# Performance work log

Hardware: AMD Instinct MI355X
Metric: run time of the kernel (lower is better)

Reference implementation:

```python
import jax, jax.numpy as jnp
import numpy as np

N = 4096      # nodes
D = 256       # in_dim == out_dim (residual forces equality)
H = 4         # n_heads
E = 131072    # edges (avg degree 32)
LN_EPS = 1e-5


def setup_inputs() -> dict:
    key = jax.random.key(0)
    ks = jax.random.split(key, 6)
    s = 1.0 / np.sqrt(D)
    node_features = jax.random.normal(ks[0], (N, D), dtype=jnp.float32)
    edge_index = jax.random.randint(ks[1], (2, E), 0, N, dtype=jnp.int64)
    in_proj_w = (jax.random.normal(ks[2], (3 * D, D), dtype=jnp.float32) * s)
    in_proj_b = jnp.zeros((3 * D,), jnp.float32)
    out_proj_w = (jax.random.normal(ks[3], (D, D), dtype=jnp.float32) * s)
    out_proj_b = jnp.zeros((D,), jnp.float32)
    proj_w = (jax.random.normal(ks[4], (D, D), dtype=jnp.float32) * s)
    proj_b = jnp.zeros((D,), jnp.float32)
    ln_gamma = jnp.ones((D,), jnp.float32)
    ln_beta = jnp.zeros((D,), jnp.float32)
    return {
        "node_features": node_features, "edge_index": edge_index,
        "in_proj_w": in_proj_w, "in_proj_b": in_proj_b,
        "out_proj_w": out_proj_w, "out_proj_b": out_proj_b,
        "proj_w": proj_w, "proj_b": proj_b,
        "ln_gamma": ln_gamma, "ln_beta": ln_beta,
    }


def _allowed_mask(edge_index, n):
    # True where attention is allowed (edges symmetrized + self loops)
    src, dst = edge_index[0], edge_index[1]
    m = jnp.zeros((n, n), dtype=bool)
    m = m.at[src, dst].set(True)
    m = m.at[dst, src].set(True)
    diag = jnp.arange(n)
    return m.at[diag, diag].set(True)


def reference(node_features, edge_index, in_proj_w, in_proj_b,
              out_proj_w, out_proj_b, proj_w, proj_b, ln_gamma, ln_beta):
    n, d = node_features.shape
    hd = d // H
    allowed = _allowed_mask(edge_index, n)

    # packed QKV projection (torch MultiheadAttention in_proj)
    qkv = node_features @ in_proj_w.T + in_proj_b          # [N, 3D]
    q, k, v = jnp.split(qkv, 3, axis=-1)
    q = q.reshape(n, H, hd).transpose(1, 0, 2)             # [H, N, hd]
    k = k.reshape(n, H, hd).transpose(1, 0, 2)
    v = v.reshape(n, H, hd).transpose(1, 0, 2)

    scores = jnp.einsum('hqd,hkd->hqk', q, k) / np.sqrt(hd)  # [H, N, N]
    scores = jnp.where(allowed[None], scores, -jnp.inf)
    attn = jax.nn.softmax(scores, axis=-1)
    ctx = jnp.einsum('hqk,hkd->hqd', attn, v)               # [H, N, hd]
    ctx = ctx.transpose(1, 0, 2).reshape(n, d)              # [N, D]
    attended = ctx @ out_proj_w.T + out_proj_b

    out = attended @ proj_w.T + proj_b                      # proj (dropout=eval identity)
    y = out + node_features                                 # residual
    mu = jnp.mean(y, axis=-1, keepdims=True)
    var = jnp.var(y, axis=-1, keepdims=True)
    return (y - mu) / jnp.sqrt(var + LN_EPS) * ln_gamma + ln_beta
```

## Files before the change

### kernel.cpp

```cpp
#include <hip/hip_runtime.h>
#include <math.h>

#define N_NODES 4096
#define DIM 256
#define HEADS 4
#define HDIM 64
#define NEDGE 131072
#define MAXNBR 256
#define MASK_WORDS 128

typedef __attribute__((ext_vector_type(8))) short short8;
typedef __attribute__((ext_vector_type(4))) float float4v;
typedef __attribute__((ext_vector_type(2))) float float2v;

__device__ inline unsigned short f2b(float f) {
    unsigned u = __float_as_uint(f);
    unsigned r = u + 0x7fffu + ((u >> 16) & 1u);
    return (unsigned short)(r >> 16);
}
__device__ inline float bl(unsigned u) { return __uint_as_float(u << 16); }
__device__ inline float bh(unsigned u) { return __uint_as_float(u & 0xffff0000u); }

__device__ inline uint4 pack8(float4 a, float4 b) {
    uint4 w;
    w.x = (unsigned)f2b(a.x) | ((unsigned)f2b(a.y) << 16);
    w.y = (unsigned)f2b(a.z) | ((unsigned)f2b(a.w) << 16);
    w.z = (unsigned)f2b(b.x) | ((unsigned)f2b(b.y) << 16);
    w.w = (unsigned)f2b(b.z) | ((unsigned)f2b(b.w) << 16);
    return w;
}

#if __has_builtin(__builtin_amdgcn_cvt_pk_f32_fp8) && __has_builtin(__builtin_amdgcn_cvt_pk_fp8_f32)
template <bool HI>
__device__ inline float2v pk8(unsigned w) {
    return __builtin_amdgcn_cvt_pk_f32_fp8((int)w, HI);
}
__device__ inline unsigned char enc8(float v) {
    return (unsigned char)(__builtin_amdgcn_cvt_pk_fp8_f32(v, v, 0, false) & 0xff);
}
#else
__device__ inline unsigned char enc8(float f) {
    unsigned u = __float_as_uint(f);
    unsigned s = (u >> 24) & 0x80u;
    float a = fabsf(f);
    if (!(a >= 0.015625f)) return (unsigned char)s;
    if (a > 448.f) return (unsigned char)(s | 0x7E);
    unsigned r = u + 0x7FFFFu + ((u >> 20) & 1u);
    unsigned e8 = ((r >> 23) & 255u) - 120u;
    unsigned m = (r >> 20) & 7u;
    if (e8 >= 15u && m == 7u) return (unsigned char)(s | 0x7E);
    return (unsigned char)(s | (e8 << 3) | m);
}
__device__ inline float d8s(unsigned b) {
    unsigned e = (b >> 3) & 15u;
    unsigned bits = ((b & 0x80u) << 24) | ((e + 120u) << 23) | ((b & 7u) << 20);
    return e ? __uint_as_float(bits) : 0.f;
}
template <bool HI>
__device__ inline float2v pk8(unsigned w) {
    unsigned x = HI ? (w >> 16) : w;
    float2v r;
    r.x = d8s(x & 255u);
    r.y = d8s((x >> 8) & 255u);
    return r;
}
#endif

__global__ __launch_bounds__(256)
void prep_kernel(const float* __restrict__ w_in,
                 const float* __restrict__ wp, const float* __restrict__ wout,
                 const float* __restrict__ bout, const float* __restrict__ bp,
                 const int* __restrict__ eidx, unsigned int* __restrict__ mask,
                 unsigned short* __restrict__ w_in_bf,
                 unsigned short* __restrict__ wc, float* __restrict__ bc) {
    const int b = blockIdx.x;
    const int tid = threadIdx.x;
    if (b < 192) {
        int t = b * 1024 + tid * 4;
        float4 v = *(const float4*)&w_in[t];
        ushort4 o;
        o.x = f2b(v.x); o.y = f2b(v.y); o.z = f2b(v.z); o.w = f2b(v.w);
        *(ushort4*)&w_in_bf[t] = o;
    } else if (b < 448) {
        int bb = b - 192;
        int i = (bb >> 4) * 16 + (tid >> 4);
        int j = (bb & 15) * 16 + (tid & 15);
        float a0 = 0.f, a1 = 0.f, a2 = 0.f, a3 = 0.f;
        for (int k = 0; k < 256; k += 4) {
            a0 = fmaf(wp[i * 256 + k + 0], wout[(k + 0) * 256 + j], a0);
            a1 = fmaf(wp[i * 256 + k + 1], wout[(k + 1) * 256 + j], a1);
            a2 = fmaf(wp[i * 256 + k + 2], wout[(k + 2) * 256 + j], a2);
            a3 = fmaf(wp[i * 256 + k + 3], wout[(k + 3) * 256 + j], a3);
        }
        wc[i * 256 + j] = f2b((a0 + a1) + (a2 + a3));
        if (bb == 0) {
            float b0 = bp[tid], b1 = 0.f, b2 = 0.f, b3 = 0.f;
            for (int k = 0; k < 256; k += 4) {
                b0 = fmaf(wp[tid * 256 + k + 0], bout[k + 0], b0);
                b1 = fmaf(wp[tid * 256 + k + 1], bout[k + 1], b1);
                b2 = fmaf(wp[tid * 256 + k + 2], bout[k + 2], b2);
                b3 = fmaf(wp[tid * 256 + k + 3], bout[k + 3], b3);
            }
            bc[tid] = (b0 + b1) + (b2 + b3);
        }
    } else {
        int t = (b - 448) * 256 + tid;
        int s = eidx[t];
        int d = eidx[NEDGE + t];
        atomicOr(&mask[s * MASK_WORDS + (d >> 5)], 1u << (d & 31));
        atomicOr(&mask[d * MASK_WORDS + (s >> 5)], 1u << (s & 31));
    }
}

__global__ __launch_bounds__(256)
void gemm_qkv(const float* __restrict__ A, const unsigned short* __restrict__ B,
              const float* __restrict__ bias,
              unsigned short* __restrict__ q_bf, unsigned char* __restrict__ kv8) {
    __shared__ unsigned short As[64 * 64];
    __shared__ unsigned short Bs[64 * 64];
    const int tid  = threadIdx.x;
    const int lane = tid & 63;
    const int wave = tid >> 6;
    const int brow = blockIdx.y * 64;
    const int bcol = blockIdx.x * 64;
    const int K = DIM;

    float4v acc[4];
#pragma unroll
    for (int t = 0; t < 4; ++t) acc[t] = (float4v){0.f, 0.f, 0.f, 0.f};

    const int quad = lane >> 4;
    const int l16  = lane & 15;

    for (int k0 = 0; k0 < K; k0 += 64) {
        __syncthreads();
#pragma unroll
        for (int it = 0; it < 2; ++it) {
            int c = it * 256 + tid;
            int row = c >> 3;
            int col = c & 7;
            int sw  = col ^ (row & 7);
            float4 a0 = *(const float4*)&A[(size_t)(brow + row) * K + k0 + col * 8];
            float4 a1 = *(const float4*)&A[(size_t)(brow + row) * K + k0 + col * 8 + 4];
            uint4 va = pack8(a0, a1);
            uint4 vb = *(const uint4*)&B[(size_t)(bcol + row) * K + k0 + col * 8];
            *(uint4*)&As[row * 64 + sw * 8] = va;
            *(uint4*)&Bs[row * 64 + sw * 8] = vb;
        }
        __syncthreads();
#pragma unroll
        for (int kk = 0; kk < 2; ++kk) {
            short8 af, bf[4];
            {
                int row = wave * 16 + l16;
                int sw = (kk * 4 + quad) ^ (row & 7);
                af = *(const short8*)&As[row * 64 + sw * 8];
            }
#pragma unroll
            for (int nt = 0; nt < 4; ++nt) {
                int row = nt * 16 + l16;
                int sw = (kk * 4 + quad) ^ (row & 7);
                bf[nt] = *(const short8*)&Bs[row * 64 + sw * 8];
            }
#pragma unroll
            for (int nt = 0; nt < 4; ++nt)
                acc[nt] = __builtin_amdgcn_mfma_f32_16x16x32_bf16(af, bf[nt], acc[nt], 0, 0, 0);
        }
    }

#pragma unroll
    for (int nt = 0; nt < 4; ++nt) {
        int colg = bcol + nt * 16 + l16;
        float bsv = bias[colg];
#pragma unroll
        for (int reg = 0; reg < 4; ++reg) {
            int rowg = brow + wave * 16 + quad * 4 + reg;
            float v = acc[nt][reg] + bsv;
            if (colg < 256)
                q_bf[(size_t)rowg * 256 + colg] = f2b(v);
            else
                kv8[(size_t)rowg * 512 + (colg - 256)] = enc8(v);
        }
    }
}

__global__ __launch_bounds__(256)
void attn_sparse_kernel(const unsigned short* __restrict__ q_bf,
                        const unsigned char* __restrict__ kv8,
                        const unsigned int* __restrict__ mask,
                        unsigned short* __restrict__ ctx) {
    __shared__ unsigned int rowmask[MASK_WORDS];
    __shared__ int cols_s[MAXNBR];
    __shared__ int count_s;

    const int tid  = threadIdx.x;
    const int wave = tid >> 6;
    const int lane = tid & 63;
    const int ng = lane >> 3;
    const int dg = lane & 7;
    const int i = blockIdx.x;
    const int h = wave;

    if (tid < MASK_WORDS) rowmask[tid] = mask[(size_t)i * MASK_WORDS + tid];

    float qf[8];
    {
        uint4 qv = *(const uint4*)&q_bf[(size_t)i * 256 + h * HDIM + dg * 8];
        qf[0] = bl(qv.x); qf[1] = bh(qv.x);
        qf[2] = bl(qv.y); qf[3] = bh(qv.y);
        qf[4] = bl(qv.z); qf[5] = bh(qv.z);
        qf[6] = bl(qv.w); qf[7] = bh(qv.w);
    }
    __syncthreads();

    if (wave == 0) {
        unsigned w0 = rowmask[lane * 2];
        unsigned w1 = rowmask[lane * 2 + 1];
        int wi = i >> 5;
        if (wi == lane * 2)     w0 |= 1u << (i & 31);
        if (wi == lane * 2 + 1) w1 |= 1u << (i & 31);
        int cnt = __popc(w0) + __popc(w1);
        int incl = cnt;
#pragma unroll
        for (int off = 1; off < 64; off <<= 1) {
            int v = __shfl_up(incl, off, 64);
            if (lane >= off) incl += v;
        }
        int c = incl - cnt;
        int total = __shfl(incl, 63, 64);
        while (w0) {
            int b = __ffs(w0) - 1;
            if (c < MAXNBR) cols_s[c] = lane * 64 + b;
            ++c; w0 &= w0 - 1u;
        }
        while (w1) {
            int b = __ffs(w1) - 1;
            if (c < MAXNBR) cols_s[c] = lane * 64 + 32 + b;
            ++c; w1 &= w1 - 1u;
        }
        if (lane == 0) count_s = total > MAXNBR ? MAXNBR : total;
    }
    __syncthreads();
    const int count = count_s;

    const unsigned char* kB = kv8 + h * HDIM + dg * 8;
    const unsigned char* vB = kv8 + 256 + h * HDIM + dg * 8;
    float a0 = 0.f, a1 = 0.f, a2 = 0.f, a3 = 0.f, a4 = 0.f, a5 = 0.f, a6 = 0.f, a7 = 0.f;
    float esum = 0.f;

    for (int t0 = 0; t0 < count; t0 += 16) {
        int tA = t0 + ng;
        int tB = t0 + 8 + ng;
        int jA = cols_s[min(tA, count - 1)];
        int jB = cols_s[min(tB, count - 1)];
        uint2 kA = *(const uint2*)&kB[(size_t)jA * 512];
        uint2 vA = *(const uint2*)&vB[(size_t)jA * 512];
        uint2 kBB = *(const uint2*)&kB[(size_t)jB * 512];
        uint2 vBB = *(const uint2*)&vB[(size_t)jB * 512];
        float2v kA0 = pk8<false>(kA.x), kA1 = pk8<true>(kA.x);
        float2v kA2 = pk8<false>(kA.y), kA3 = pk8<true>(kA.y);
        float2v kB0 = pk8<false>(kBB.x), kB1 = pk8<true>(kBB.x);
        float2v kB2 = pk8<false>(kBB.y), kB3 = pk8<true>(kBB.y);
        float sA = qf[0] * kA0.x + qf[1] * kA0.y + qf[2] * kA1.x + qf[3] * kA1.y
                 + qf[4] * kA2.x + qf[5] * kA2.y + qf[6] * kA3.x + qf[7] * kA3.y;
        float sB = qf[0] * kB0.x + qf[1] * kB0.y + qf[2] * kB1.x + qf[3] * kB1.y
                 + qf[4] * kB2.x + qf[5] * kB2.y + qf[6] * kB3.x + qf[7] * kB3.y;
        sA += __shfl_xor(sA, 1, 64);  sB += __shfl_xor(sB, 1, 64);
        sA += __shfl_xor(sA, 2, 64);  sB += __shfl_xor(sB, 2, 64);
        sA += __shfl_xor(sA, 4, 64);  sB += __shfl_xor(sB, 4, 64);
        float eA = (tA < count) ? __expf(sA * 0.125f) : 0.f;
        float eB = (tB < count) ? __expf(sB * 0.125f) : 0.f;
        esum += eA + eB;
        float2v vA0 = pk8<false>(vA.x), vA1 = pk8<true>(vA.x);
        float2v vA2 = pk8<false>(vA.y), vA3 = pk8<true>(vA.y);
        float2v vB0 = pk8<false>(vBB.x), vB1 = pk8<true>(vBB.x);
        float2v vB2 = pk8<false>(vBB.y), vB3 = pk8<true>(vBB.y);
        a0 = fmaf(eA, vA0.x, a0); a1 = fmaf(eA, vA0.y, a1);
        a2 = fmaf(eA, vA1.x, a2); a3 = fmaf(eA, vA1.y, a3);
        a4 = fmaf(eA, vA2.x, a4); a5 = fmaf(eA, vA2.y, a5);
        a6 = fmaf(eA, vA3.x, a6); a7 = fmaf(eA, vA3.y, a7);
        a0 = fmaf(eB, vB0.x, a0); a1 = fmaf(eB, vB0.y, a1);
        a2 = fmaf(eB, vB1.x, a2); a3 = fmaf(eB, vB1.y, a3);
        a4 = fmaf(eB, vB2.x, a4); a5 = fmaf(eB, vB2.y, a5);
        a6 = fmaf(eB, vB3.x, a6); a7 = fmaf(eB, vB3.y, a7);
    }
#pragma unroll
    for (int off = 8; off <= 32; off <<= 1) {
        esum += __shfl_xor(esum, off, 64);
        a0 += __shfl_xor(a0, off, 64); a1 += __shfl_xor(a1, off, 64);
        a2 += __shfl_xor(a2, off, 64); a3 += __shfl_xor(a3, off, 64);
        a4 += __shfl_xor(a4, off, 64); a5 += __shfl_xor(a5, off, 64);
        a6 += __shfl_xor(a6, off, 64); a7 += __shfl_xor(a7, off, 64);
    }
    if (ng == 0) {
        float inv = 1.0f / esum;
        uint4 w;
        w.x = (unsigned)f2b(a0 * inv) | ((unsigned)f2b(a1 * inv) << 16);
        w.y = (unsigned)f2b(a2 * inv) | ((unsigned)f2b(a3 * inv) << 16);
        w.z = (unsigned)f2b(a4 * inv) | ((unsigned)f2b(a5 * inv) << 16);
        w.w = (unsigned)f2b(a6 * inv) | ((unsigned)f2b(a7 * inv) << 16);
        *(uint4*)&ctx[(size_t)i * DIM + h * HDIM + dg * 8] = w;
    }
}

__global__ __launch_bounds__(256)
void gemm_ln(const unsigned short* __restrict__ A, const unsigned short* __restrict__ B,
             const float* __restrict__ bc, const float* __restrict__ x,
             const float* __restrict__ gamma, const float* __restrict__ beta,
             float* __restrict__ out) {
    __shared__ unsigned short As[16 * 64];
    __shared__ unsigned short Bs[256 * 64];
    __shared__ float redS[16][4];
    __shared__ float redQ[16][4];
    const int tid  = threadIdx.x;
    const int lane = tid & 63;
    const int wave = tid >> 6;
    const int brow = blockIdx.x * 16;
    const int K = DIM;

    float4v acc[4];
#pragma unroll
    for (int t = 0; t < 4; ++t) acc[t] = (float4v){0.f, 0.f, 0.f, 0.f};

    const int quad = lane >> 4;
    const int l16  = lane & 15;

    for (int k0 = 0; k0 < K; k0 += 64) {
        __syncthreads();
#pragma unroll
        for (int it = 0; it < 8; ++it) {
            int c = it * 256 + tid;
            int row = c >> 3;
            int col = c & 7;
            int sw  = col ^ (row & 7);
            uint4 vb = *(const uint4*)&B[(size_t)row * K + k0 + col * 8];
            *(uint4*)&Bs[row * 64 + sw * 8] = vb;
        }
        if (tid < 128) {
            int row = tid >> 3;
            int col = tid & 7;
            int sw  = col ^ (row & 7);
            uint4 va = *(const uint4*)&A[(size_t)(brow + row) * K + k0 + col * 8];
            *(uint4*)&As[row * 64 + sw * 8] = va;
        }
        __syncthreads();
#pragma unroll
        for (int kk = 0; kk < 2; ++kk) {
            short8 af, bf[4];
            {
                int row = l16;
                int sw = (kk * 4 + quad) ^ (row & 7);
                af = *(const short8*)&As[row * 64 + sw * 8];
            }
#pragma unroll
            for (int nt = 0; nt < 4; ++nt) {
                int row = wave * 64 + nt * 16 + l16;
                int sw = (kk * 4 + quad) ^ (row & 7);
                bf[nt] = *(const short8*)&Bs[row * 64 + sw * 8];
            }
#pragma unroll
            for (int nt = 0; nt < 4; ++nt)
                acc[nt] = __builtin_amdgcn_mfma_f32_16x16x32_bf16(af, bf[nt], acc[nt], 0, 0, 0);
        }
    }

    float vals[4][4];
    float ps[4] = {0.f, 0.f, 0.f, 0.f};
    float pq[4] = {0.f, 0.f, 0.f, 0.f};
#pragma unroll
    for (int nt = 0; nt < 4; ++nt) {
        int colg = wave * 64 + nt * 16 + l16;
        float bcv = bc[colg];
#pragma unroll
        for (int reg = 0; reg < 4; ++reg) {
            int rowg = brow + quad * 4 + reg;
            float v = acc[nt][reg] + bcv + x[(size_t)rowg * 256 + colg];
            vals[nt][reg] = v;
            ps[reg] += v;
            pq[reg] += v * v;
        }
    }
#pragma unroll
    for (int off = 1; off <= 8; off <<= 1) {
#pragma unroll
        for (int reg = 0; reg < 4; ++reg) {
            ps[reg] += __shfl_xor(ps[reg], off, 64);
            pq[reg] += __shfl_xor(pq[reg], off, 64);
        }
    }
    if (l16 == 0) {
#pragma unroll
        for (int reg = 0; reg < 4; ++reg) {
            redS[quad * 4 + reg][wave] = ps[reg];
            redQ[quad * 4 + reg][wave] = pq[reg];
        }
    }
    __syncthreads();
#pragma unroll
    for (int reg = 0; reg < 4; ++reg) {
        int rowl = quad * 4 + reg;
        float s = redS[rowl][0] + redS[rowl][1] + redS[rowl][2] + redS[rowl][3];
        float q = redQ[rowl][0] + redQ[rowl][1] + redQ[rowl][2] + redQ[rowl][3];
        float mean = s * (1.f / 256.f);
        float var = q * (1.f / 256.f) - mean * mean;
        float rstd = rsqrtf(var + 1e-5f);
        int rowg = brow + rowl;
#pragma unroll
        for (int nt = 0; nt < 4; ++nt) {
            int colg = wave * 64 + nt * 16 + l16;
            out[(size_t)rowg * 256 + colg] =
                (vals[nt][reg] - mean) * rstd * gamma[colg] + beta[colg];
        }
    }
}

extern "C" void kernel_launch(void* const* d_in, const int* in_sizes, int n_in,
                              void* d_out, int out_size, void* d_ws, size_t ws_size,
                              hipStream_t stream) {
    const float* x      = (const float*)d_in[0];
    const int*   eidx   = (const int*)d_in[1];
    const float* w_in   = (const float*)d_in[2];
    const float* b_in   = (const float*)d_in[3];
    const float* w_out  = (const float*)d_in[4];
    const float* b_out  = (const float*)d_in[5];
    const float* w_p    = (const float*)d_in[6];
    const float* b_p    = (const float*)d_in[7];
    const float* gamma  = (const float*)d_in[8];
    const float* beta   = (const float*)d_in[9];
    float* out = (float*)d_out;

    char* ws = (char*)d_ws;
    unsigned int*   mask    = (unsigned int*)(ws + 0);
    unsigned short* q_bf    = (unsigned short*)(ws + 2097152);
    unsigned char*  kv8     = (unsigned char*)(ws + 4194304);
    unsigned short* ctx_bf  = (unsigned short*)(ws + 6291456);
    unsigned short* w_in_bf = (unsigned short*)(ws + 8388608);
    unsigned short* wc_bf   = (unsigned short*)(ws + 8781824);
    float*          bc      = (float*)(ws + 8912896);

    (void)hipMemsetAsync(mask, 0, N_NODES * MASK_WORDS * 4, stream);
    prep_kernel<<<960, 256, 0, stream>>>(w_in, w_p, w_out, b_out, b_p, eidx, mask,
                                         w_in_bf, wc_bf, bc);
    {
        dim3 grid(768 / 64, N_NODES / 64);
        gemm_qkv<<<grid, 256, 0, stream>>>(x, w_in_bf, b_in, q_bf, kv8);
    }
    attn_sparse_kernel<<<N_NODES, 256, 0, stream>>>(q_bf, kv8, mask, ctx_bf);
    gemm_ln<<<N_NODES / 16, 256, 0, stream>>>(ctx_bf, wc_bf, bc, x, gamma, beta, out);
}
```

Before: 132.3 us.

## Fuse QKV GEMM into prep kernel and convert weights to bf16 inline

Merges the weight-prep kernel and the QKV projection GEMM into one launch. Blocks are split by index into GEMM tiles, combined-weight computation and edge-mask atomics. The GEMM now reads fp32 in_proj weights and packs them to bf16 while loading, so the separate bf16 weight buffer and its conversion pass go away. The attention kernel also reads its mask words straight from global memory instead of staging them in shared memory, which removes a barrier. The cost is that each GEMM tile converts weights redundantly and loads twice the weight bytes.

```diff
diff --git a/kernel.cpp b/kernel.cpp
--- a/kernel.cpp
+++ b/kernel.cpp
@@ -67,22 +67,86 @@
 #endif
 
 __global__ __launch_bounds__(256)
-void prep_kernel(const float* __restrict__ w_in,
+void mega_kernel(const float* __restrict__ x, const float* __restrict__ w_in,
+                 const float* __restrict__ b_in,
                  const float* __restrict__ wp, const float* __restrict__ wout,
                  const float* __restrict__ bout, const float* __restrict__ bp,
                  const int* __restrict__ eidx, unsigned int* __restrict__ mask,
-                 unsigned short* __restrict__ w_in_bf,
+                 unsigned short* __restrict__ q_bf, unsigned char* __restrict__ kv8,
                  unsigned short* __restrict__ wc, float* __restrict__ bc) {
     const int b = blockIdx.x;
     const int tid = threadIdx.x;
-    if (b < 192) {
-        int t = b * 1024 + tid * 4;
-        float4 v = *(const float4*)&w_in[t];
-        ushort4 o;
-        o.x = f2b(v.x); o.y = f2b(v.y); o.z = f2b(v.z); o.w = f2b(v.w);
-        *(ushort4*)&w_in_bf[t] = o;
-    } else if (b < 448) {
-        int bb = b - 192;
+
+    if (b < 768) {
+        __shared__ unsigned short As[64 * 64];
+        __shared__ unsigned short Bs[64 * 64];
+        const int lane = tid & 63;
+        const int wave = tid >> 6;
+        const int bx = b % 12;
+        const int by = b / 12;
+        const int brow = by * 64;
+        const int bcol = bx * 64;
+        const int K = DIM;
+
+        float4v acc[4];
+#pragma unroll
+        for (int t = 0; t < 4; ++t) acc[t] = (float4v){0.f, 0.f, 0.f, 0.f};
+
+        const int quad = lane >> 4;
+        const int l16  = lane & 15;
+
+        for (int k0 = 0; k0 < K; k0 += 64) {
+            __syncthreads();
+#pragma unroll
+            for (int it = 0; it < 2; ++it) {
+                int c = it * 256 + tid;
+                int row = c >> 3;
+                int col = c & 7;
+                int sw  = col ^ (row & 7);
+                float4 a0 = *(const float4*)&x[(size_t)(brow + row) * K + k0 + col * 8];
+                float4 a1 = *(const float4*)&x[(size_t)(brow + row) * K + k0 + col * 8 + 4];
+                float4 b0 = *(const float4*)&w_in[(size_t)(bcol + row) * K + k0 + col * 8];
+                float4 b1 = *(const float4*)&w_in[(size_t)(bcol + row) * K + k0 + col * 8 + 4];
+                *(uint4*)&As[row * 64 + sw * 8] = pack8(a0, a1);
+                *(uint4*)&Bs[row * 64 + sw * 8] = pack8(b0, b1);
+            }
+            __syncthreads();
+#pragma unroll
+            for (int kk = 0; kk < 2; ++kk) {
+                short8 af, bf[4];
+                {
+                    int row = wave * 16 + l16;
+                    int sw = (kk * 4 + quad) ^ (row & 7);
+                    af = *(const short8*)&As[row * 64 + sw * 8];
+                }
+#pragma unroll
+                for (int nt = 0; nt < 4; ++nt) {
+                    int row = nt * 16 + l16;
+                    int sw = (kk * 4 + quad) ^ (row & 7);
+                    bf[nt] = *(const short8*)&Bs[row * 64 + sw * 8];
+                }
+#pragma unroll
+                for (int nt = 0; nt < 4; ++nt)
+                    acc[nt] = __builtin_amdgcn_mfma_f32_16x16x32_bf16(af, bf[nt], acc[nt], 0, 0, 0);
+            }
+        }
+
+#pragma unroll
+        for (int nt = 0; nt < 4; ++nt) {
+            int colg = bcol + nt * 16 + l16;
+            float bsv = b_in[colg];
+#pragma unroll
+            for (int reg = 0; reg < 4; ++reg) {
+                int rowg = brow + wave * 16 + quad * 4 + reg;
+                float v = acc[nt][reg] + bsv;
+                if (colg < 256)
+                    q_bf[(size_t)rowg * 256 + colg] = f2b(v);
+                else
+                    kv8[(size_t)rowg * 512 + (colg - 256)] = enc8(v);
+            }
+        }
+    } else if (b < 1024) {
+        int bb = b - 768;
         int i = (bb >> 4) * 16 + (tid >> 4);
         int j = (bb & 15) * 16 + (tid & 15);
         float a0 = 0.f, a1 = 0.f, a2 = 0.f, a3 = 0.f;
@@ -104,83 +168,11 @@
             bc[tid] = (b0 + b1) + (b2 + b3);
         }
     } else {
-        int t = (b - 448) * 256 + tid;
+        int t = (b - 1024) * 256 + tid;
         int s = eidx[t];
         int d = eidx[NEDGE + t];
         atomicOr(&mask[s * MASK_WORDS + (d >> 5)], 1u << (d & 31));
         atomicOr(&mask[d * MASK_WORDS + (s >> 5)], 1u << (s & 31));
-    }
-}
-
-__global__ __launch_bounds__(256)
-void gemm_qkv(const float* __restrict__ A, const unsigned short* __restrict__ B,
-              const float* __restrict__ bias,
-              unsigned short* __restrict__ q_bf, unsigned char* __restrict__ kv8) {
-    __shared__ unsigned short As[64 * 64];
-    __shared__ unsigned short Bs[64 * 64];
-    const int tid  = threadIdx.x;
-    const int lane = tid & 63;
-    const int wave = tid >> 6;
-    const int brow = blockIdx.y * 64;
-    const int bcol = blockIdx.x * 64;
-    const int K = DIM;
-
-    float4v acc[4];
-#pragma unroll
-    for (int t = 0; t < 4; ++t) acc[t] = (float4v){0.f, 0.f, 0.f, 0.f};
-
-    const int quad = lane >> 4;
-    const int l16  = lane & 15;
-
-    for (int k0 = 0; k0 < K; k0 += 64) {
-        __syncthreads();
-#pragma unroll
-        for (int it = 0; it < 2; ++it) {
-            int c = it * 256 + tid;
-            int row = c >> 3;
-            int col = c & 7;
-            int sw  = col ^ (row & 7);
-            float4 a0 = *(const float4*)&A[(size_t)(brow + row) * K + k0 + col * 8];
-            float4 a1 = *(const float4*)&A[(size_t)(brow + row) * K + k0 + col * 8 + 4];
-            uint4 va = pack8(a0, a1);
-            uint4 vb = *(const uint4*)&B[(size_t)(bcol + row) * K + k0 + col * 8];
-            *(uint4*)&As[row * 64 + sw * 8] = va;
-            *(uint4*)&Bs[row * 64 + sw * 8] = vb;
-        }
-        __syncthreads();
-#pragma unroll
-        for (int kk = 0; kk < 2; ++kk) {
-            short8 af, bf[4];
-            {
-                int row = wave * 16 + l16;
-                int sw = (kk * 4 + quad) ^ (row & 7);
-                af = *(const short8*)&As[row * 64 + sw * 8];
-            }
-#pragma unroll
-            for (int nt = 0; nt < 4; ++nt) {
-                int row = nt * 16 + l16;
-                int sw = (kk * 4 + quad) ^ (row & 7);
-                bf[nt] = *(const short8*)&Bs[row * 64 + sw * 8];
-            }
-#pragma unroll
-            for (int nt = 0; nt < 4; ++nt)
-                acc[nt] = __builtin_amdgcn_mfma_f32_16x16x32_bf16(af, bf[nt], acc[nt], 0, 0, 0);
-        }
-    }
-
-#pragma unroll
-    for (int nt = 0; nt < 4; ++nt) {
-        int colg = bcol + nt * 16 + l16;
-        float bsv = bias[colg];
-#pragma unroll
-        for (int reg = 0; reg < 4; ++reg) {
-            int rowg = brow + wave * 16 + quad * 4 + reg;
-            float v = acc[nt][reg] + bsv;
-            if (colg < 256)
-                q_bf[(size_t)rowg * 256 + colg] = f2b(v);
-            else
-                kv8[(size_t)rowg * 512 + (colg - 256)] = enc8(v);
-        }
     }
 }
 
@@ -189,7 +181,6 @@
                         const unsigned char* __restrict__ kv8,
                         const unsigned int* __restrict__ mask,
                         unsigned short* __restrict__ ctx) {
-    __shared__ unsigned int rowmask[MASK_WORDS];
     __shared__ int cols_s[MAXNBR];
     __shared__ int count_s;
 
@@ -201,8 +192,6 @@
     const int i = blockIdx.x;
     const int h = wave;
 
-    if (tid < MASK_WORDS) rowmask[tid] = mask[(size_t)i * MASK_WORDS + tid];
-
     float qf[8];
     {
         uint4 qv = *(const uint4*)&q_bf[(size_t)i * 256 + h * HDIM + dg * 8];
@@ -211,11 +200,11 @@
         qf[4] = bl(qv.z); qf[5] = bh(qv.z);
         qf[6] = bl(qv.w); qf[7] = bh(qv.w);
     }
-    __syncthreads();
 
     if (wave == 0) {
-        unsigned w0 = rowmask[lane * 2];
-        unsigned w1 = rowmask[lane * 2 + 1];
+        uint2 mw = *(const uint2*)&mask[(size_t)i * MASK_WORDS + lane * 2];
+        unsigned w0 = mw.x;
+        unsigned w1 = mw.y;
         int wi = i >> 5;
         if (wi == lane * 2)     w0 |= 1u << (i & 31);
         if (wi == lane * 2 + 1) w1 |= 1u << (i & 31);
@@ -434,17 +423,12 @@
     unsigned short* q_bf    = (unsigned short*)(ws + 2097152);
     unsigned char*  kv8     = (unsigned char*)(ws + 4194304);
     unsigned short* ctx_bf  = (unsigned short*)(ws + 6291456);
-    unsigned short* w_in_bf = (unsigned short*)(ws + 8388608);
-    unsigned short* wc_bf   = (unsigned short*)(ws + 8781824);
-    float*          bc      = (float*)(ws + 8912896);
+    unsigned short* wc_bf   = (unsigned short*)(ws + 8388608);
+    float*          bc      = (float*)(ws + 8519680);
 
     (void)hipMemsetAsync(mask, 0, N_NODES * MASK_WORDS * 4, stream);
-    prep_kernel<<<960, 256, 0, stream>>>(w_in, w_p, w_out, b_out, b_p, eidx, mask,
-                                         w_in_bf, wc_bf, bc);
-    {
-        dim3 grid(768 / 64, N_NODES / 64);
-        gemm_qkv<<<grid, 256, 0, stream>>>(x, w_in_bf, b_in, q_bf, kv8);
-    }
+    mega_kernel<<<1536, 256, 0, stream>>>(x, w_in, b_in, w_p, w_out, b_out, b_p,
+                                          eidx, mask, q_bf, kv8, wc_bf, bc);
     attn_sparse_kernel<<<N_NODES, 256, 0, stream>>>(q_bf, kv8, mask, ctx_bf);
     gemm_ln<<<N_NODES / 16, 256, 0, stream>>>(ctx_bf, wc_bf, bc, x, gamma, beta, out);
 }
```

Measured after the change: 125.7 us. 1.05x faster.
